# Kernel tuning notes

Hardware: AMD Instinct MI355X
Metric: run time of the kernel (lower is better)

## Reference

```python
import jax, jax.numpy as jnp
import numpy as np


def conv2d(x, w, b=None, pad=1):
    out = jax.lax.conv_general_dilated(
        x, w, window_strides=(1, 1), padding=[(pad, pad), (pad, pad)],
        dimension_numbers=('NCHW', 'OIHW', 'NCHW'))
    if b is not None:
        out = out + b[None, :, None, None]
    return out


def instance_norm(x, eps=1e-5):
    # InstanceNorm2d (no affine): normalize each (b, c) plane over H, W (biased var)
    mu = x.mean(axis=(2, 3), keepdims=True)
    var = x.var(axis=(2, 3), keepdims=True)
    return (x - mu) * jax.lax.rsqrt(var + eps)


def setup_inputs() -> dict:
    key = jax.random.key(0)
    ks = jax.random.split(key, 16)
    B, C, H, W, F, L, NH = 4, 64, 128, 128, 5, 512, 128
    s = lambda i, shape: jax.random.normal(ks[i], shape, jnp.float32) * 0.05
    return {
        'x': jax.random.normal(ks[0], (B, C, H, W), jnp.float32),
        'segmap': jax.random.randint(ks[1], (B, F, H, W), 0, 2).astype(jnp.float32),
        'codes_vector': jax.random.normal(ks[2], (B, F, L), jnp.float32),
        'mask': jax.random.randint(ks[3], (B, 3, H, W), 0, 2).astype(jnp.float32),
        'fc_w': s(4, (F, L, L)),           # per facial-feature Linear weight [out,in]
        'fc_b': s(5, (F, L)),
        'conv_gamma_w': s(6, (C, L, 3, 3)),
        'conv_gamma_b': s(7, (C,)),
        'conv_beta_w': s(8, (C, L, 3, 3)),
        'conv_beta_b': s(9, (C,)),
        'spade_shared_w': s(10, (NH, 3, 3, 3)),
        'spade_shared_b': s(11, (NH,)),
        'spade_gamma_w': s(12, (C, NH, 3, 3)),
        'spade_gamma_b': s(13, (C,)),
        'spade_beta_w': s(14, (C, NH, 3, 3)),
        'spade_beta_b': s(15, (C,)),
        'blending_gamma': jnp.zeros((1,), jnp.float32),
        'blending_beta': jnp.zeros((1,), jnp.float32),
    }


def reference(x, segmap, codes_vector, mask, fc_w, fc_b,
              conv_gamma_w, conv_gamma_b, conv_beta_w, conv_beta_b,
              spade_shared_w, spade_shared_b, spade_gamma_w, spade_gamma_b,
              spade_beta_w, spade_beta_b, blending_gamma, blending_beta):
    B, C, H, W = x.shape
    F_ = segmap.shape[1]
    x_norm = instance_norm(x)  # add_noise=False branch
    seg_bool = segmap > 0      # [B, F, H, W]; segmap already at x resolution
    # per-region style vector: mu[b,f,:] = relu(Linear_f(codes_vector[b,f]))
    mu = jax.nn.relu(jnp.einsum('bfl,fkl->bfk', codes_vector, fc_w) + fc_b[None])  # [B,F,L]
    # vectorized replacement of the per-(b,j) masked_scatter_ loop: later regions overwrite
    L = mu.shape[-1]
    middle = jnp.zeros((B, L, H, W), x.dtype)
    for j in range(F_):
        middle = jnp.where(seg_bool[:, j][:, None], mu[:, j][:, :, None, None], middle)
    gamma_avg = conv2d(middle, conv_gamma_w, conv_gamma_b)
    beta_avg = conv2d(middle, conv_beta_w, conv_beta_b)
    # SPADE on the (already full-res) mask
    actv = jax.nn.relu(conv2d(mask, spade_shared_w, spade_shared_b))
    gamma_spade = conv2d(actv, spade_gamma_w, spade_gamma_b)
    beta_spade = conv2d(actv, spade_beta_w, spade_beta_b)
    ga = jax.nn.sigmoid(blending_gamma)[0]
    ba = jax.nn.sigmoid(blending_beta)[0]
    gamma_final = ga * gamma_avg + (1.0 - ga) * gamma_spade
    beta_final = ba * beta_avg + (1.0 - ba) * beta_spade
    return x_norm * (1.0 + gamma_final) + beta_final
```

## Files before the change

### kernel.cpp

```cpp
#include <hip/hip_runtime.h>
#include <math.h>

#define HD 128
#define WD 128
#define LD 512
#define NHD 128
#define HW (HD*WD)

typedef _Float16 half8 __attribute__((ext_vector_type(8)));
typedef float floatx4 __attribute__((ext_vector_type(4)));
typedef float floatx16 __attribute__((ext_vector_type(16)));

#define OFF_MU      0
#define OFF_TG      10240
#define OFF_TB      24064
#define OFF_MEAN    37888
#define OFF_RSTD    38144
#define OFF_CT      38400
#define OFF_W3      628224
#define OFF_ACTVH   701952
#define OFF_IDX_BYTES ((size_t)(701952 + 4194304) * 4)

__device__ constexpr int mloff(int k) {
    return ((k / 9) * 3 + ((k % 9) / 3)) * 66 + ((k % 9) % 3);
}

__global__ void __launch_bounds__(256) k_pre1(
    const float* __restrict__ x, const float* __restrict__ segmap,
    const float* __restrict__ codes, const float* __restrict__ mask,
    const float* __restrict__ fc_w, const float* __restrict__ fc_b,
    const float* __restrict__ cgw, const float* __restrict__ cbw,
    const float* __restrict__ sgw, const float* __restrict__ sbw,
    const float* __restrict__ ssw, const float* __restrict__ ssb,
    const float* __restrict__ bgam, const float* __restrict__ bbet,
    float* __restrict__ mu, float* __restrict__ CT, _Float16* __restrict__ W3,
    unsigned char* __restrict__ idxm, float* __restrict__ meanp,
    float* __restrict__ rstdp, _Float16* __restrict__ actvh) {
    int bid = blockIdx.x, t = threadIdx.x;

    if (bid < 256) {
        __shared__ float sl[64][37];
        int tbl = bid >> 7, cq4 = bid & 127;
        const float* src = tbl ? cbw : cgw;
        int o = t >> 2, q = t & 3;
        const float* sp = src + (size_t)o * 4608 + cq4 * 36 + q * 9;
        #pragma unroll
        for (int j = 0; j < 9; ++j) sl[o][q * 9 + j] = sp[j];
        __syncthreads();
        int o_w = t & 63, s = t >> 6;
        float* dst = CT + (size_t)tbl * 294912;
        #pragma unroll
        for (int tap = 0; tap < 9; ++tap)
            dst[((size_t)tap * 512 + cq4 * 4 + s) * 64 + o_w] = sl[o_w][s * 9 + tap];
        return;
    }
    if (bid < 288) {
        __shared__ _Float16 sl2[32][145];
        int e2 = bid - 256;
        int tbl = e2 >> 4, ocg = (e2 >> 3) & 1, chq = e2 & 7;
        const float* src = tbl ? sbw : sgw;
        float blg = 1.f / (1.f + __expf(-bgam[0]));
        float blb = 1.f / (1.f + __expf(-bbet[0]));
        float scale = tbl ? (1.f - blb) : (1.f - blg);
        int oc_r = t >> 3, i = t & 7;
        const float* sp = src + (size_t)(ocg * 32 + oc_r) * 1152 + chq * 144 + i * 18;
        #pragma unroll
        for (int j = 0; j < 18; ++j) sl2[oc_r][i * 18 + j] = (_Float16)(sp[j] * scale);
        __syncthreads();
        for (int s = 0; s < 3; ++s) {
            int task = s * 256 + t;
            if (task < 576) {
                int tap = task >> 6, ln = task & 63;
                int lo = ln & 31, hb = ln >> 5;
                half8 hv;
                #pragma unroll
                for (int j = 0; j < 8; ++j)
                    hv[j] = sl2[lo][(hb * 8 + j) * 9 + tap];
                *(half8*)(W3 + ((((size_t)tbl * 9 + tap) * 2 + ocg) * 8 + chq) * 512
                          + ln * 8) = hv;
            }
        }
        return;
    }
    if (bid < 448) {
        __shared__ float cs[LD];
        int sid = bid - 288;
        int bf = sid >> 3, chunk = sid & 7, f = bf % 5;
        cs[t] = codes[(size_t)bf * LD + t];
        cs[t + 256] = codes[(size_t)bf * LD + t + 256];
        __syncthreads();
        int row = t >> 2, lane4 = t & 3;
        int k = chunk * 64 + row;
        const float* wrow = fc_w + ((size_t)f * LD + k) * LD;
        float acc = 0.f;
        for (int j = 0; j < 32; ++j) {
            int l = lane4 * 4 + j * 16;
            float4 wv = *(const float4*)(wrow + l);
            float4 cv = *(const float4*)(cs + l);
            acc += wv.x * cv.x + wv.y * cv.y + wv.z * cv.z + wv.w * cv.w;
        }
        acc += __shfl_xor(acc, 1);
        acc += __shfl_xor(acc, 2);
        if (lane4 == 0)
            mu[(size_t)bf * LD + k] = fmaxf(acc + fc_b[f * LD + k], 0.f);
        return;
    }
    if (bid < 704) {
        int pid = (bid - 448) * 256 + t;
        int b = pid >> 14, p = pid & 16383;
        unsigned char v = 5;
        for (int f = 0; f < 5; ++f)
            if (segmap[((size_t)b * 5 + f) * HW + p] > 0.f) v = (unsigned char)f;
        idxm[pid] = v;
        return;
    }
    if (bid < 960) {
        __shared__ float as[4], as2[4];
        int plane = bid - 704;
        const float* xp = x + (size_t)plane * HW;
        float s = 0.f, s2 = 0.f;
        for (int j = 0; j < 16; ++j) {
            float4 v = *(const float4*)(xp + ((size_t)t + j * 256) * 4);
            s += v.x + v.y + v.z + v.w;
            s2 += v.x * v.x + v.y * v.y + v.z * v.z + v.w * v.w;
        }
        for (int off = 32; off; off >>= 1) { s += __shfl_xor(s, off); s2 += __shfl_xor(s2, off); }
        int wid = t >> 6;
        if ((t & 63) == 0) { as[wid] = s; as2[wid] = s2; }
        __syncthreads();
        if (t == 0) {
            s = as[0] + as[1] + as[2] + as[3];
            s2 = as2[0] + as2[1] + as2[2] + as2[3];
            float m = s * (1.f / HW);
            float var = s2 * (1.f / HW) - m * m;
            meanp[plane] = m;
            rstdp[plane] = rsqrtf(var + 1e-5f);
        }
        return;
    }
    {
        __shared__ float ml[3][3][66];
        __shared__ _Float16 Bs2[4096];
        __shared__ _Float16 Cbuf[8192];
        int sid = bid - 960;
        int xh = sid & 1, h = (sid >> 1) & 127, b = sid >> 8;
        int w0 = xh * 64;
        for (int e = t; e < 594; e += 256) {
            int col = e % 66; int rc = e / 66; int ky = rc % 3; int c = rc / 3;
            int y = h - 1 + ky; int xx = w0 - 1 + col;
            float v = 0.f;
            if ((unsigned)y < 128u && (unsigned)xx < 128u)
                v = mask[(((size_t)b * 3 + c) * HD + y) * WD + xx];
            ml[c][ky][col] = v;
        }
        for (int e = t; e < 512; e += 256) {
            int ks = e >> 8, hb = (e >> 7) & 1, oc = e & 127;
            int kb = ks * 16 + hb * 8;
            half8 hv;
            #pragma unroll
            for (int j = 0; j < 8; ++j)
                hv[j] = (kb + j < 27) ? (_Float16)ssw[oc * 27 + kb + j] : (_Float16)0.f;
            *(half8*)(&Bs2[(size_t)e * 8]) = hv;
        }
        __syncthreads();
        int lane = t & 63, wv = t >> 6;
        int l31 = lane & 31, hb = lane >> 5;
        int oc = wv * 32 + l31;
        const float* mlf = &ml[0][0][0];
        floatx16 acc[2];
        #pragma unroll
        for (int i = 0; i < 16; ++i) { acc[0][i] = 0.f; acc[1][i] = 0.f; }
        #pragma unroll
        for (int ks = 0; ks < 2; ++ks) {
            half8 bfrag = *(const half8*)(&Bs2[((ks * 2 + hb) * 128 + oc) * 8]);
            #pragma unroll
            for (int mf = 0; mf < 2; ++mf) {
                int px = mf * 32 + l31;
                half8 a;
                #pragma unroll
                for (int j = 0; j < 8; ++j) {
                    int k_lo = ks * 16 + j;
                    int k_hi = k_lo + 8;
                    float v;
                    if (k_hi < 27)
                        v = mlf[(hb ? mloff(18 + (k_lo - (k_lo / 9) * 9) + ((k_lo / 9) == 0 ? -9 : -9)) : 0) + 0];
                    if (k_hi < 27)
                        v = hb ? mlf[mloff(k_hi) + px] : mlf[mloff(k_lo) + px];
                    else
                        v = hb ? 0.f : mlf[mloff(k_lo) + px];
                    a[j] = (_Float16)v;
                }
                acc[mf] = __builtin_amdgcn_mfma_f32_32x32x16_f16(a, bfrag, acc[mf], 0, 0, 0);
            }
        }
        float bv = ssb[oc];
        #pragma unroll
        for (int mf = 0; mf < 2; ++mf)
            #pragma unroll
            for (int q = 0; q < 4; ++q)
                #pragma unroll
                for (int r = 0; r < 4; ++r) {
                    int px = mf * 32 + 8 * q + 4 * hb + r;
                    Cbuf[px * 128 + oc] = (_Float16)fmaxf(acc[mf][q * 4 + r] + bv, 0.f);
                }
        __syncthreads();
        for (int e = t; e < 1024; e += 256) {
            int px = e >> 4, ch8 = e & 15;
            *(half8*)(actvh + (((size_t)b * HD + h) * WD + w0 + px) * NHD + ch8 * 8) =
                *(const half8*)(&Cbuf[px * 128 + ch8 * 8]);
        }
    }
}

__global__ void __launch_bounds__(1024) k_pre2(
    const float* __restrict__ mu, const float* __restrict__ CT,
    float* __restrict__ Tg, float* __restrict__ Tb) {
    int bid = blockIdx.x;
    int tap = bid % 9; int bf6 = bid / 9;
    int f = bf6 % 6, b = bf6 / 6;
    int t = threadIdx.x;
    size_t base = (size_t)bid * 64;
    if (f == 5) {
        if (t < 64) { Tg[base + t] = 0.f; Tb[base + t] = 0.f; }
        return;
    }
    __shared__ float ms[LD];
    __shared__ float red[2][16][64];
    if (t < 512) ms[t] = mu[(((size_t)b * 5 + f) << 9) + t];
    __syncthreads();
    int o = t & 63, cq = t >> 6;
    const float* cg = CT + ((size_t)tap * 512 + cq * 32) * 64 + o;
    const float* cb = cg + 294912;
    float ag = 0.f, ab = 0.f;
    #pragma unroll 8
    for (int i = 0; i < 32; ++i) {
        float m = ms[cq * 32 + i];
        ag = fmaf(m, cg[(size_t)i * 64], ag);
        ab = fmaf(m, cb[(size_t)i * 64], ab);
    }
    red[0][cq][o] = ag; red[1][cq][o] = ab;
    __syncthreads();
    if (t < 128) {
        int tb2 = t >> 6, oo = t & 63;
        float s = 0.f;
        #pragma unroll
        for (int i = 0; i < 16; ++i) s += red[tb2][i][oo];
        (tb2 ? Tb : Tg)[base + oo] = s;
    }
}

__global__ void __launch_bounds__(256, 3)
k_main(const float* __restrict__ x, const _Float16* __restrict__ actvh,
       const unsigned char* __restrict__ idxm,
       const float* __restrict__ Tg, const float* __restrict__ Tb,
       const _Float16* __restrict__ W3,
       const float* __restrict__ meanp, const float* __restrict__ rstdp,
       const float* __restrict__ cgb, const float* __restrict__ cbb,
       const float* __restrict__ sgb, const float* __restrict__ sbb,
       const float* __restrict__ bgam, const float* __restrict__ bbet,
       float* __restrict__ out) {
    __shared__ _Float16 As[4 * 66 * 64];
    __shared__ _Float16 T2f[8192];
    __shared__ unsigned char ir[4][68];
    int t = threadIdx.x;

    int gid = blockIdx.x;
    int logical = (gid & 7) * 64 + (gid >> 3);
    int c64 = logical & 1, rp = (logical >> 1) & 63, b = logical >> 7;
    int w0 = c64 * 64, y0 = rp * 2;

    int lane = t & 63, w = t >> 6;
    int row_l = w >> 1, c32 = (w & 1) * 32;
    int l31 = lane & 31, hi = lane >> 5;

    float ga = 1.f / (1.f + __expf(-bgam[0]));
    float ba = 1.f / (1.f + __expf(-bbet[0]));

    for (int e = t; e < 264; e += 256) {
        int r = e / 66, j = e % 66;
        int y = y0 - 1 + r, xx = w0 + j - 1;
        ir[r][j] = ((unsigned)y < 128u && (unsigned)xx < 128u)
                       ? idxm[((size_t)b << 14) + (y << 7) + xx] : (unsigned char)5;
    }
    for (int task = t; task < 1024; task += 256) {
        int tbl = task >> 9, rem = task & 511;
        int ocs = rem >> 8, ks = (rem >> 6) & 3, ln = rem & 63;
        int oc = ocs * 32 + (ln & 31);
        int kb = ks * 16 + (ln >> 5) * 8;
        const float* Tsrc = tbl ? Tb : Tg;
        float sc = tbl ? ba : ga;
        half8 hv;
        #pragma unroll
        for (int j = 0; j < 8; ++j) {
            int k = kb + j;
            int f = (k * 57) >> 9;
            int tp = k - f * 9;
            float v = (f < 6) ? Tsrc[(((size_t)b * 6 + f) * 9 + tp) * 64 + oc] * sc : 0.f;
            hv[j] = (_Float16)v;
        }
        *(half8*)(&T2f[task * 8]) = hv;
    }

    floatx16 accg[2], accb[2];
    #pragma unroll
    for (int i = 0; i < 16; ++i) {
        accg[0][i] = 0.f; accg[1][i] = 0.f;
        accb[0][i] = 0.f; accb[1][i] = 0.f;
    }

    for (int half = 0; half < 2; ++half) {
        int ch0 = half * 64;
        for (int e = t; e < 2112; e += 256) {
            int ch8 = e & 7, col = (e >> 3) % 66, row = e / 528;
            int y = y0 - 1 + row, xx = w0 - 1 + col;
            uint4 v = make_uint4(0u, 0u, 0u, 0u);
            if ((unsigned)y < 128u && (unsigned)xx < 128u)
                v = *(const uint4*)(actvh + ((((size_t)b * HD + y) * WD + xx) << 7)
                                    + ch0 + ch8 * 8);
            *(uint4*)(&As[((row * 66 + col) << 6) + ((ch8 ^ (col & 7)) << 3)]) = v;
        }
        __syncthreads();
        #pragma unroll
        for (int tap = 0; tap < 9; ++tap) {
            int ky = tap / 3, kx = tap - ky * 3;
            int colA = c32 + l31 + kx;
            int rowA = row_l + ky;
            int abase = (rowA * 66 + colA) << 6;
            int sw = colA & 7;
            const _Float16* wg0 = W3 + (((size_t)tap * 2 + 0) * 8 + half * 4) * 512
                                  + lane * 8;
            const _Float16* wg1 = W3 + (((size_t)tap * 2 + 1) * 8 + half * 4) * 512
                                  + lane * 8;
            #pragma unroll
            for (int ks = 0; ks < 4; ++ks) {
                half8 a = *(const half8*)(&As[abase + (((ks * 2 + hi) ^ sw) << 3)]);
                half8 bg0 = *(const half8*)(wg0 + ks * 512);
                half8 bg1 = *(const half8*)(wg1 + ks * 512);
                half8 bb0 = *(const half8*)(wg0 + 73728 + ks * 512);
                half8 bb1 = *(const half8*)(wg1 + 73728 + ks * 512);
                accg[0] = __builtin_amdgcn_mfma_f32_32x32x16_f16(a, bg0, accg[0], 0, 0, 0);
                accg[1] = __builtin_amdgcn_mfma_f32_32x32x16_f16(a, bg1, accg[1], 0, 0, 0);
                accb[0] = __builtin_amdgcn_mfma_f32_32x32x16_f16(a, bb0, accb[0], 0, 0, 0);
                accb[1] = __builtin_amdgcn_mfma_f32_32x32x16_f16(a, bb1, accb[1], 0, 0, 0);
            }
        }
        __syncthreads();
    }

    unsigned long long fpack = 0ull;
    #pragma unroll
    for (int ky = 0; ky < 3; ++ky)
        #pragma unroll
        for (int kx = 0; kx < 3; ++kx) {
            unsigned long long f = ir[row_l + ky][c32 + l31 + kx];
            fpack |= f << ((ky * 3 + kx) * 6);
        }
    #pragma unroll
    for (int ks = 0; ks < 4; ++ks) {
        int kb = ks * 16 + hi * 8;
        half8 a1;
        #pragma unroll
        for (int j = 0; j < 8; ++j) {
            int k = kb + j;
            int f = (k * 57) >> 9;
            int tp6 = (k - f * 9) * 6;
            int fp = (int)((fpack >> tp6) & 63ull);
            a1[j] = (fp == f) ? (_Float16)1.0f : (_Float16)0.0f;
        }
        #pragma unroll
        for (int ocg = 0; ocg < 2; ++ocg) {
            half8 bg = *(const half8*)(&T2f[((ocg * 4 + ks) * 64 + lane) * 8]);
            half8 bb = *(const half8*)(&T2f[(((2 + ocg) * 4 + ks) * 64 + lane) * 8]);
            accg[ocg] = __builtin_amdgcn_mfma_f32_32x32x16_f16(a1, bg, accg[ocg], 0, 0, 0);
            accb[ocg] = __builtin_amdgcn_mfma_f32_32x32x16_f16(a1, bb, accb[ocg], 0, 0, 0);
        }
    }

    #pragma unroll
    for (int ocg = 0; ocg < 2; ++ocg) {
        int oc = ocg * 32 + l31;
        int plane = b * 64 + oc;
        float mean = meanp[plane], rstd = rstdp[plane];
        float gbias = ga * cgb[oc] + (1.f - ga) * sgb[oc];
        float bbias = ba * cbb[oc] + (1.f - ba) * sbb[oc];
        size_t rowoff = (size_t)plane * HW + (y0 + row_l) * WD + w0 + c32;
        const float* xrow = x + rowoff;
        float* orow = out + rowoff;
        #pragma unroll
        for (int q = 0; q < 4; ++q) {
            int p0 = 8 * q + 4 * hi;
            float4 xv = *(const float4*)(xrow + p0);
            float xa[4] = {xv.x, xv.y, xv.z, xv.w};
            float res[4];
            #pragma unroll
            for (int r2 = 0; r2 < 4; ++r2) {
                float gf = accg[ocg][q * 4 + r2] + gbias;
                float bf = accb[ocg][q * 4 + r2] + bbias;
                res[r2] = (xa[r2] - mean) * rstd * (1.f + gf) + bf;
            }
            *(float4*)(orow + p0) = make_float4(res[0], res[1], res[2], res[3]);
        }
    }
}

extern "C" void kernel_launch(void* const* d_in, const int* in_sizes, int n_in,
                              void* d_out, int out_size, void* d_ws, size_t ws_size,
                              hipStream_t stream) {
    const float* x      = (const float*)d_in[0];
    const float* segmap = (const float*)d_in[1];
    const float* codes  = (const float*)d_in[2];
    const float* mask   = (const float*)d_in[3];
    const float* fc_w   = (const float*)d_in[4];
    const float* fc_b   = (const float*)d_in[5];
    const float* cgw    = (const float*)d_in[6];
    const float* cgb    = (const float*)d_in[7];
    const float* cbw    = (const float*)d_in[8];
    const float* cbb    = (const float*)d_in[9];
    const float* ssw    = (const float*)d_in[10];
    const float* ssb    = (const float*)d_in[11];
    const float* sgw    = (const float*)d_in[12];
    const float* sgb    = (const float*)d_in[13];
    const float* sbw    = (const float*)d_in[14];
    const float* sbb    = (const float*)d_in[15];
    const float* bgam   = (const float*)d_in[16];
    const float* bbet   = (const float*)d_in[17];
    float* out = (float*)d_out;

    float* wsf = (float*)d_ws;
    float* mu    = wsf + OFF_MU;
    float* Tg    = wsf + OFF_TG;
    float* Tb    = wsf + OFF_TB;
    float* meanp = wsf + OFF_MEAN;
    float* rstdp = wsf + OFF_RSTD;
    float* CT    = wsf + OFF_CT;
    _Float16* W3    = (_Float16*)(wsf + OFF_W3);
    _Float16* actvh = (_Float16*)(wsf + OFF_ACTVH);
    unsigned char* idxm = (unsigned char*)d_ws + OFF_IDX_BYTES;

    k_pre1<<<1984, 256, 0, stream>>>(x, segmap, codes, mask, fc_w, fc_b,
                                     cgw, cbw, sgw, sbw, ssw, ssb, bgam, bbet,
                                     mu, CT, W3, idxm, meanp, rstdp, actvh);
    k_pre2<<<216, 1024, 0, stream>>>(mu, CT, Tg, Tb);
    k_main<<<512, 256, 0, stream>>>(x, actvh, idxm, Tg, Tb, W3,
                                    meanp, rstdp, cgb, cbb, sgb, sbb,
                                    bgam, bbet, out);
}
```

Measured before the change: 178.1 us.

## Retile main SPADE conv to 4-row tiles with LDS double-buffered weights

k_main now processes a 4-row by 64-column tile with 512 threads (256 blocks). All 128 actv channels for the tile are staged into LDS in a single pass, so there is only one fill instead of two half-channel passes. Per-tap gamma/beta weights are prefetched into registers two steps ahead and double-buffered through LDS. Each wave reuses one B fragment across two 32-pixel A fragments, so weight traffic is no longer read directly from global memory per MFMA. The trade-off is much larger LDS use (about 150KB) and fewer, bigger blocks, which lowers occupancy and grid parallelism on a GPU with many CUs.

```diff
diff --git a/kernel.cpp b/kernel.cpp
--- a/kernel.cpp
+++ b/kernel.cpp
@@ -8,7 +8,6 @@
 #define HW (HD*WD)
 
 typedef _Float16 half8 __attribute__((ext_vector_type(8)));
-typedef float floatx4 __attribute__((ext_vector_type(4)));
 typedef float floatx16 __attribute__((ext_vector_type(16)));
 
 #define OFF_MU      0
@@ -183,8 +182,6 @@
                     int k_hi = k_lo + 8;
                     float v;
                     if (k_hi < 27)
-                        v = mlf[(hb ? mloff(18 + (k_lo - (k_lo / 9) * 9) + ((k_lo / 9) == 0 ? -9 : -9)) : 0) + 0];
-                    if (k_hi < 27)
                         v = hb ? mlf[mloff(k_hi) + px] : mlf[mloff(k_lo) + px];
                     else
                         v = hb ? 0.f : mlf[mloff(k_lo) + px];
@@ -249,7 +246,7 @@
     }
 }
 
-__global__ void __launch_bounds__(256, 3)
+__global__ void __launch_bounds__(512, 2)
 k_main(const float* __restrict__ x, const _Float16* __restrict__ actvh,
        const unsigned char* __restrict__ idxm,
        const float* __restrict__ Tg, const float* __restrict__ Tb,
@@ -259,30 +256,51 @@
        const float* __restrict__ sgb, const float* __restrict__ sbb,
        const float* __restrict__ bgam, const float* __restrict__ bbet,
        float* __restrict__ out) {
-    __shared__ _Float16 As[4 * 66 * 64];
+    __shared__ _Float16 As[50688];
+    __shared__ _Float16 Bs[16384];
     __shared__ _Float16 T2f[8192];
-    __shared__ unsigned char ir[4][68];
+    __shared__ unsigned char ir[6][66];
     int t = threadIdx.x;
 
     int gid = blockIdx.x;
-    int logical = (gid & 7) * 64 + (gid >> 3);
-    int c64 = logical & 1, rp = (logical >> 1) & 63, b = logical >> 7;
-    int w0 = c64 * 64, y0 = rp * 2;
+    int logical = (gid & 7) * 32 + (gid >> 3);
+    int c64 = logical & 1, rp = (logical >> 1) & 31, b = logical >> 6;
+    int w0 = c64 * 64, y0 = rp * 4;
 
     int lane = t & 63, w = t >> 6;
-    int row_l = w >> 1, c32 = (w & 1) * 32;
+    int mh = w >> 1, nh = w & 1;
     int l31 = lane & 31, hi = lane >> 5;
+
+    int seg = t >> 5, lo32 = t & 31;
+    int tbl_s = seg >> 3, ocg_s = (seg >> 2) & 1, kq_s = seg & 3;
 
     float ga = 1.f / (1.f + __expf(-bgam[0]));
     float ba = 1.f / (1.f + __expf(-bbet[0]));
 
-    for (int e = t; e < 264; e += 256) {
-        int r = e / 66, j = e % 66;
+    uint4 bpA0, bpA1, bpB0, bpB1;
+    {
+        const _Float16* gp = W3 + ((((size_t)tbl_s * 9 + 0) * 2 + ocg_s) * 8
+                                   + 0 * 4 + kq_s) * 512 + lo32 * 16;
+        bpA0 = *(const uint4*)gp; bpA1 = *(const uint4*)(gp + 8);
+    }
+
+    if (t < 396) {
+        int r = t / 66, j = t - r * 66;
         int y = y0 - 1 + r, xx = w0 + j - 1;
         ir[r][j] = ((unsigned)y < 128u && (unsigned)xx < 128u)
                        ? idxm[((size_t)b << 14) + (y << 7) + xx] : (unsigned char)5;
     }
-    for (int task = t; task < 1024; task += 256) {
+
+    for (int e = t; e < 6336; e += 512) {
+        int ch8 = e & 15, col = (e >> 4) % 66, row = e / 1056;
+        int y = y0 - 1 + row, xx = w0 - 1 + col;
+        uint4 v = make_uint4(0u, 0u, 0u, 0u);
+        if ((unsigned)y < 128u && (unsigned)xx < 128u)
+            v = *(const uint4*)(actvh + ((((size_t)b * HD + y) * WD + xx) << 7) + ch8 * 8);
+        *(uint4*)(&As[((row * 66 + col) << 7) + ((ch8 ^ (col & 7)) << 3)]) = v;
+    }
+
+    for (int task = t; task < 1024; task += 512) {
         int tbl = task >> 9, rem = task & 511;
         int ocs = rem >> 8, ks = (rem >> 6) & 3, ln = rem & 63;
         int oc = ocs * 32 + (ln & 31);
@@ -301,6 +319,17 @@
         *(half8*)(&T2f[task * 8]) = hv;
     }
 
+    {
+        const _Float16* gp = W3 + ((((size_t)tbl_s * 9 + 1) * 2 + ocg_s) * 8
+                                   + 0 * 4 + kq_s) * 512 + lo32 * 16;
+        bpB0 = *(const uint4*)gp; bpB1 = *(const uint4*)(gp + 8);
+    }
+    {
+        _Float16* lp = Bs + seg * 512 + lo32 * 16;
+        *(uint4*)lp = bpA0; *(uint4*)(lp + 8) = bpA1;
+    }
+    __syncthreads();
+
     floatx16 accg[2], accb[2];
     #pragma unroll
     for (int i = 0; i < 16; ++i) {
@@ -308,97 +337,93 @@
         accb[0][i] = 0.f; accb[1][i] = 0.f;
     }
 
-    for (int half = 0; half < 2; ++half) {
-        int ch0 = half * 64;
-        for (int e = t; e < 2112; e += 256) {
-            int ch8 = e & 7, col = (e >> 3) % 66, row = e / 528;
-            int y = y0 - 1 + row, xx = w0 - 1 + col;
-            uint4 v = make_uint4(0u, 0u, 0u, 0u);
-            if ((unsigned)y < 128u && (unsigned)xx < 128u)
-                v = *(const uint4*)(actvh + ((((size_t)b * HD + y) * WD + xx) << 7)
-                                    + ch0 + ch8 * 8);
-            *(uint4*)(&As[((row * 66 + col) << 6) + ((ch8 ^ (col & 7)) << 3)]) = v;
-        }
-        __syncthreads();
-        #pragma unroll
-        for (int tap = 0; tap < 9; ++tap) {
-            int ky = tap / 3, kx = tap - ky * 3;
-            int colA = c32 + l31 + kx;
-            int rowA = row_l + ky;
-            int abase = (rowA * 66 + colA) << 6;
-            int sw = colA & 7;
-            const _Float16* wg0 = W3 + (((size_t)tap * 2 + 0) * 8 + half * 4) * 512
-                                  + lane * 8;
-            const _Float16* wg1 = W3 + (((size_t)tap * 2 + 1) * 8 + half * 4) * 512
-                                  + lane * 8;
-            #pragma unroll
-            for (int ks = 0; ks < 4; ++ks) {
-                half8 a = *(const half8*)(&As[abase + (((ks * 2 + hi) ^ sw) << 3)]);
-                half8 bg0 = *(const half8*)(wg0 + ks * 512);
-                half8 bg1 = *(const half8*)(wg1 + ks * 512);
-                half8 bb0 = *(const half8*)(wg0 + 73728 + ks * 512);
-                half8 bb1 = *(const half8*)(wg1 + 73728 + ks * 512);
-                accg[0] = __builtin_amdgcn_mfma_f32_32x32x16_f16(a, bg0, accg[0], 0, 0, 0);
-                accg[1] = __builtin_amdgcn_mfma_f32_32x32x16_f16(a, bg1, accg[1], 0, 0, 0);
-                accb[0] = __builtin_amdgcn_mfma_f32_32x32x16_f16(a, bb0, accb[0], 0, 0, 0);
-                accb[1] = __builtin_amdgcn_mfma_f32_32x32x16_f16(a, bb1, accb[1], 0, 0, 0);
-            }
-        }
-        __syncthreads();
-    }
-
-    unsigned long long fpack = 0ull;
+    int cur = 0;
+    for (int i = 0; i < 18; ++i) {
+        if (i + 1 < 18) {
+            _Float16* lp = Bs + (cur ^ 1) * 8192 + seg * 512 + lo32 * 16;
+            if ((i + 1) & 1) { *(uint4*)lp = bpB0; *(uint4*)(lp + 8) = bpB1; }
+            else             { *(uint4*)lp = bpA0; *(uint4*)(lp + 8) = bpA1; }
+        }
+        if (i + 2 < 18) {
+            int i2 = i + 2, hf2 = i2 / 9, tap2 = i2 - hf2 * 9;
+            const _Float16* gp = W3 + ((((size_t)tbl_s * 9 + tap2) * 2 + ocg_s) * 8
+                                       + hf2 * 4 + kq_s) * 512 + lo32 * 16;
+            if (i & 1) { bpB0 = *(const uint4*)gp; bpB1 = *(const uint4*)(gp + 8); }
+            else       { bpA0 = *(const uint4*)gp; bpA1 = *(const uint4*)(gp + 8); }
+        }
+        int hf = i / 9, tap = i - hf * 9;
+        int ky = tap / 3, kx = tap - ky * 3;
+        int colA = l31 + kx;
+        int ra = ((mh + ky) * 66 + colA) << 7;
+        int sw = colA & 7;
+        const _Float16* Bcur = Bs + cur * 8192 + (nh << 11) + (lane << 3);
+        #pragma unroll
+        for (int ks = 0; ks < 4; ++ks) {
+            int gsel = (((hf * 8 + ks * 2) + hi) ^ sw) << 3;
+            half8 a0 = *(const half8*)(&As[ra + gsel]);
+            half8 a1 = *(const half8*)(&As[ra + (32 << 7) + gsel]);
+            half8 bgv = *(const half8*)(Bcur + (ks << 9));
+            half8 bbv = *(const half8*)(Bcur + 4096 + (ks << 9));
+            accg[0] = __builtin_amdgcn_mfma_f32_32x32x16_f16(a0, bgv, accg[0], 0, 0, 0);
+            accg[1] = __builtin_amdgcn_mfma_f32_32x32x16_f16(a1, bgv, accg[1], 0, 0, 0);
+            accb[0] = __builtin_amdgcn_mfma_f32_32x32x16_f16(a0, bbv, accb[0], 0, 0, 0);
+            accb[1] = __builtin_amdgcn_mfma_f32_32x32x16_f16(a1, bbv, accb[1], 0, 0, 0);
+        }
+        __syncthreads();
+        cur ^= 1;
+    }
+
+    unsigned long long fp0 = 0ull, fp1 = 0ull;
     #pragma unroll
     for (int ky = 0; ky < 3; ++ky)
         #pragma unroll
         for (int kx = 0; kx < 3; ++kx) {
-            unsigned long long f = ir[row_l + ky][c32 + l31 + kx];
-            fpack |= f << ((ky * 3 + kx) * 6);
+            int sh = (ky * 3 + kx) * 6;
+            fp0 |= (unsigned long long)ir[mh + ky][l31 + kx] << sh;
+            fp1 |= (unsigned long long)ir[mh + ky][32 + l31 + kx] << sh;
         }
     #pragma unroll
     for (int ks = 0; ks < 4; ++ks) {
         int kb = ks * 16 + hi * 8;
-        half8 a1;
+        half8 bg = *(const half8*)(&T2f[((nh * 4 + ks) * 64 + lane) * 8]);
+        half8 bb = *(const half8*)(&T2f[(((2 + nh) * 4 + ks) * 64 + lane) * 8]);
+        half8 a0, a1;
         #pragma unroll
         for (int j = 0; j < 8; ++j) {
             int k = kb + j;
             int f = (k * 57) >> 9;
             int tp6 = (k - f * 9) * 6;
-            int fp = (int)((fpack >> tp6) & 63ull);
-            a1[j] = (fp == f) ? (_Float16)1.0f : (_Float16)0.0f;
-        }
-        #pragma unroll
-        for (int ocg = 0; ocg < 2; ++ocg) {
-            half8 bg = *(const half8*)(&T2f[((ocg * 4 + ks) * 64 + lane) * 8]);
-            half8 bb = *(const half8*)(&T2f[(((2 + ocg) * 4 + ks) * 64 + lane) * 8]);
-            accg[ocg] = __builtin_amdgcn_mfma_f32_32x32x16_f16(a1, bg, accg[ocg], 0, 0, 0);
-            accb[ocg] = __builtin_amdgcn_mfma_f32_32x32x16_f16(a1, bb, accb[ocg], 0, 0, 0);
-        }
-    }
-
+            a0[j] = ((int)((fp0 >> tp6) & 63ull) == f) ? (_Float16)1.0f : (_Float16)0.0f;
+            a1[j] = ((int)((fp1 >> tp6) & 63ull) == f) ? (_Float16)1.0f : (_Float16)0.0f;
+        }
+        accg[0] = __builtin_amdgcn_mfma_f32_32x32x16_f16(a0, bg, accg[0], 0, 0, 0);
+        accg[1] = __builtin_amdgcn_mfma_f32_32x32x16_f16(a1, bg, accg[1], 0, 0, 0);
+        accb[0] = __builtin_amdgcn_mfma_f32_32x32x16_f16(a0, bb, accb[0], 0, 0, 0);
+        accb[1] = __builtin_amdgcn_mfma_f32_32x32x16_f16(a1, bb, accb[1], 0, 0, 0);
+    }
+
+    int oc = nh * 32 + l31;
+    int plane = b * 64 + oc;
+    float mean = meanp[plane], rstd = rstdp[plane];
+    float gbias = ga * cgb[oc] + (1.f - ga) * sgb[oc];
+    float bbias = ba * cbb[oc] + (1.f - ba) * sbb[oc];
+    int row = y0 + mh;
     #pragma unroll
-    for (int ocg = 0; ocg < 2; ++ocg) {
-        int oc = ocg * 32 + l31;
-        int plane = b * 64 + oc;
-        float mean = meanp[plane], rstd = rstdp[plane];
-        float gbias = ga * cgb[oc] + (1.f - ga) * sgb[oc];
-        float bbias = ba * cbb[oc] + (1.f - ba) * sbb[oc];
-        size_t rowoff = (size_t)plane * HW + (y0 + row_l) * WD + w0 + c32;
-        const float* xrow = x + rowoff;
-        float* orow = out + rowoff;
+    for (int mi = 0; mi < 2; ++mi) {
+        size_t rowoff = (size_t)plane * HW + (size_t)row * WD + w0 + mi * 32;
         #pragma unroll
         for (int q = 0; q < 4; ++q) {
             int p0 = 8 * q + 4 * hi;
-            float4 xv = *(const float4*)(xrow + p0);
+            float4 xv = *(const float4*)(x + rowoff + p0);
             float xa[4] = {xv.x, xv.y, xv.z, xv.w};
             float res[4];
             #pragma unroll
             for (int r2 = 0; r2 < 4; ++r2) {
-                float gf = accg[ocg][q * 4 + r2] + gbias;
-                float bf = accb[ocg][q * 4 + r2] + bbias;
+                float gf = (mi ? accg[1][q * 4 + r2] : accg[0][q * 4 + r2]) + gbias;
+                float bf = (mi ? accb[1][q * 4 + r2] : accb[0][q * 4 + r2]) + bbias;
                 res[r2] = (xa[r2] - mean) * rstd * (1.f + gf) + bf;
             }
-            *(float4*)(orow + p0) = make_float4(res[0], res[1], res[2], res[3]);
+            *(float4*)(out + rowoff + p0) = make_float4(res[0], res[1], res[2], res[3]);
         }
     }
 }
@@ -441,7 +466,7 @@
                                      cgw, cbw, sgw, sbw, ssw, ssb, bgam, bbet,
                                      mu, CT, W3, idxm, meanp, rstdp, actvh);
     k_pre2<<<216, 1024, 0, stream>>>(mu, CT, Tg, Tb);
-    k_main<<<512, 256, 0, stream>>>(x, actvh, idxm, Tg, Tb, W3,
+    k_main<<<256, 512, 0, stream>>>(x, actvh, idxm, Tg, Tb, W3,
                                     meanp, rstdp, cgb, cbb, sgb, sbb,
                                     bgam, bbet, out);
 }
```

New measurement: 154.1 us. 1.16x faster.
